# Kernel optimization log

Measured on AMD Instinct MI355X. Metric: run time of the kernel, lower is better.

Reference implementation:

```python
import jax, jax.numpy as jnp
import numpy as np

NEG_SLOPE = 0.2  # PyG GATConv default negative_slope
EPS = 1e-16


def gat_conv(x, src, dst, num_nodes, W, att_src, att_dst, bias, concat):
    """PyG-style GATConv (eval mode, no dropout). att_*: [H, C]."""
    H, C = att_src.shape
    h = (x @ W).reshape(num_nodes, H, C)                      # [N,H,C]
    a_s = jnp.einsum('nhc,hc->nh', h, att_src)                # [N,H]
    a_d = jnp.einsum('nhc,hc->nh', h, att_dst)                # [N,H]
    e = jax.nn.leaky_relu(a_s[src] + a_d[dst], NEG_SLOPE)     # [E,H]
    # segment softmax over edges grouped by destination node
    m = jax.lax.stop_gradient(jax.ops.segment_max(e, dst, num_segments=num_nodes))
    ex = jnp.exp(e - m[dst])
    denom = jax.ops.segment_sum(ex, dst, num_segments=num_nodes)
    alpha = ex / (denom[dst] + EPS)                           # [E,H]
    msg = h[src] * alpha[:, :, None]                          # [E,H,C]
    out = jax.ops.segment_sum(msg, dst, num_segments=num_nodes)  # [N,H,C]
    out = out.reshape(num_nodes, H * C) if concat else out.mean(axis=1)
    return out + bias


def setup_inputs() -> dict:
    key = jax.random.key(0)
    ks = jax.random.split(key, 12)
    N, E = 65536, 1310720
    IN, HID, OUT, HEADS = 768, 128, 2, 8
    C1 = HID // HEADS  # 16
    s = 0.05
    return {
        'x': jax.random.normal(ks[0], (N, IN), jnp.float32),
        'edge_index': jax.random.randint(ks[1], (2, E), 0, N, jnp.int64),
        'W1': jax.random.normal(ks[2], (IN, HEADS * C1), jnp.float32) * s,
        'att_src1': jax.random.normal(ks[3], (HEADS, C1), jnp.float32) * s,
        'att_dst1': jax.random.normal(ks[4], (HEADS, C1), jnp.float32) * s,
        'b1': jnp.zeros((HID,), jnp.float32),
        'Wp': jax.random.normal(ks[5], (IN, HID), jnp.float32) * s,
        'bp': jnp.zeros((HID,), jnp.float32),
        'W2': jax.random.normal(ks[6], (HID, OUT), jnp.float32) * s,
        'att_src2': jax.random.normal(ks[7], (1, OUT), jnp.float32) * s,
        'att_dst2': jax.random.normal(ks[8], (1, OUT), jnp.float32) * s,
        'b2': jnp.zeros((OUT,), jnp.float32),
    }


def reference(x, edge_index, W1, att_src1, att_dst1, b1, Wp, bp, W2, att_src2, att_dst2, b2):
    N = x.shape[0]
    loops = jnp.arange(N, dtype=edge_index.dtype)  # add_self_loops=True
    src = jnp.concatenate([edge_index[0], loops])
    dst = jnp.concatenate([edge_index[1], loops])
    # eval mode: dropout is identity
    h1 = gat_conv(x, src, dst, N, W1, att_src1, att_dst1, b1, concat=True)
    h = jax.nn.elu(h1 + x @ Wp + bp)  # residual projection + ELU
    return gat_conv(h, src, dst, N, W2, att_src2, att_dst2, b2, concat=False)
```

## Files before the change

### kernel.cpp

```cpp
#include <hip/hip_runtime.h>
#include <hip/hip_bf16.h>
#include <math.h>

#define NEG_SLOPE 0.2f

typedef __attribute__((ext_vector_type(8))) short short8;
typedef __attribute__((ext_vector_type(4))) float float4v;

__device__ __forceinline__ unsigned f2bf(float f) {
  unsigned u = __builtin_bit_cast(unsigned, f);
  return (u + 0x7fffu + ((u >> 16) & 1u)) >> 16;
}
__device__ __forceinline__ float bflo(unsigned u) {
  return __builtin_bit_cast(float, u << 16);
}
__device__ __forceinline__ float bfhi(unsigned u) {
  return __builtin_bit_cast(float, u & 0xffff0000u);
}
__device__ __forceinline__ unsigned cvtpk(float lo, float hi) {
  unsigned r;
  asm("v_cvt_pk_bf16_f32 %0, %1, %2" : "=v"(r) : "v"(lo), "v"(hi));
  return r;
}
__device__ __forceinline__ void gl2lds16(const void* g, void* l) {
  __builtin_amdgcn_global_load_lds(
      (const __attribute__((address_space(1))) unsigned*)g,
      (__attribute__((address_space(3))) unsigned*)l, 16, 0, 0);
}

__global__ __launch_bounds__(256) void convert_w(const float* __restrict__ W1,
                                                 const float* __restrict__ Wp,
                                                 short* __restrict__ Wt) {
  int k = blockIdx.x;
  int c = threadIdx.x;
  float v = (c < 128) ? W1[k * 128 + c] : Wp[k * 128 + (c - 128)];
  Wt[(size_t)c * 768 + k] = (short)f2bf(v);
}

__global__ __launch_bounds__(256, 4) void gemm_mfma(
    const float* __restrict__ x, const short* __restrict__ Wt,
    float* __restrict__ proj, unsigned* __restrict__ h1bf) {
  __shared__ short As[2][2048];
  __shared__ short Bs[2][8192];
  const int tid = threadIdx.x;
  const int w = tid >> 6, l = tid & 63;
  const int l15 = l & 15, l4 = l >> 4;
  const int row0 = blockIdx.x * 64;

  const float* xsrc = x + (size_t)(row0 + (tid >> 2)) * 768 + (tid & 3) * 8;
  const int awoff = (tid >> 2) * 64 + (((tid & 3) ^ ((tid >> 3) & 3)) << 4);
  const int aoff = l15 * 64 + ((l4 ^ ((l15 >> 1) & 3)) << 4);

  const char* bg[4];
#pragma unroll
  for (int i = 0; i < 4; i++) {
    int c = w * 64 + i * 16 + (l >> 2);
    int q = (l & 3) ^ ((l >> 3) & 3);
    bg[i] = (const char*)Wt + (size_t)c * 1536 + q * 16;
  }
  const int pc = l4 ^ ((l15 >> 1) & 3);

  float4v acc[4][4] = {};

  auto loadA = [&](int t, float4& r0, float4& r1) {
    const float* p = xsrc + t * 32;
    r0 = *(const float4*)p;
    r1 = *(const float4*)(p + 4);
  };
  auto writeA = [&](short* asb, const float4& r0, const float4& r1) {
    uint4 pk;
    pk.x = cvtpk(r0.x, r0.y);
    pk.y = cvtpk(r0.z, r0.w);
    pk.z = cvtpk(r1.x, r1.y);
    pk.w = cvtpk(r1.z, r1.w);
    *(uint4*)((char*)asb + awoff) = pk;
  };
  auto stageB = [&](short* bsb, int t) {
    gl2lds16(bg[0] + t * 64, (char*)bsb + w * 4096 + 0 * 1024);
    gl2lds16(bg[1] + t * 64, (char*)bsb + w * 4096 + 1 * 1024);
    gl2lds16(bg[2] + t * 64, (char*)bsb + w * 4096 + 2 * 1024);
    gl2lds16(bg[3] + t * 64, (char*)bsb + w * 4096 + 3 * 1024);
  };
  auto compute = [&](const short* asb, const short* bsb) {
    short8 afr[4];
#pragma unroll
    for (int rt = 0; rt < 4; rt++)
      afr[rt] = *(const short8*)((const char*)asb + rt * 1024 + aoff);
#pragma unroll
    for (int ct = 0; ct < 4; ct++) {
      short8 bfr =
          *(const short8*)((const char*)bsb + (w * 64 + ct * 16 + l15) * 64 + pc * 16);
#pragma unroll
      for (int rt = 0; rt < 4; rt++)
        acc[rt][ct] =
            __builtin_amdgcn_mfma_f32_16x16x32_bf16(afr[rt], bfr, acc[rt][ct], 0, 0, 0);
    }
  };

  float4 r0, r1;
  loadA(0, r0, r1);
  stageB(Bs[0], 0);
  writeA(As[0], r0, r1);
  __syncthreads();
  for (int t = 0; t < 24; t += 2) {
    loadA(t + 1, r0, r1);
    stageB(Bs[1], t + 1);
    compute(As[0], Bs[0]);
    writeA(As[1], r0, r1);
    __syncthreads();
    if (t + 2 < 24) {
      loadA(t + 2, r0, r1);
      stageB(Bs[0], t + 2);
    }
    compute(As[1], Bs[1]);
    if (t + 2 < 24) writeA(As[0], r0, r1);
    __syncthreads();
  }

  const int colbase = w * 64;
  if (w < 2) {
#pragma unroll
    for (int ct = 0; ct < 4; ct++) {
      const int c = colbase + ct * 16 + l15;
#pragma unroll
      for (int rt = 0; rt < 4; rt++) {
#pragma unroll
        for (int r = 0; r < 4; r++) {
          const int R = row0 + rt * 16 + l4 * 4 + r;
          unsigned u = f2bf(acc[rt][ct][r]);
          unsigned up = __shfl_xor(u, 1);
          if ((l15 & 1) == 0) h1bf[(size_t)R * 64 + (c >> 1)] = u | (up << 16);
        }
      }
    }
  } else {
#pragma unroll
    for (int ct = 0; ct < 4; ct++) {
      const int c = colbase - 128 + ct * 16 + l15;
#pragma unroll
      for (int rt = 0; rt < 4; rt++) {
#pragma unroll
        for (int r = 0; r < 4; r++) {
          const int R = row0 + rt * 16 + l4 * 4 + r;
          proj[(size_t)R * 128 + c] = acc[rt][ct][r];
        }
      }
    }
  }
}

__global__ __launch_bounds__(256) void attn1b(const uint4* __restrict__ h1bf4,
                                              const float* __restrict__ att_src1,
                                              const float* __restrict__ att_dst1,
                                              float* __restrict__ a_s1,
                                              float* __restrict__ a_d1) {
  const int t = blockIdx.x * 256 + threadIdx.x;
  const int n = t >> 3, h = t & 7;
  uint4 q0 = h1bf4[(size_t)n * 16 + h * 2];
  uint4 q1 = h1bf4[(size_t)n * 16 + h * 2 + 1];
  float v[16];
  v[0] = bflo(q0.x); v[1] = bfhi(q0.x); v[2] = bflo(q0.y); v[3] = bfhi(q0.y);
  v[4] = bflo(q0.z); v[5] = bfhi(q0.z); v[6] = bflo(q0.w); v[7] = bfhi(q0.w);
  v[8] = bflo(q1.x); v[9] = bfhi(q1.x); v[10] = bflo(q1.y); v[11] = bfhi(q1.y);
  v[12] = bflo(q1.z); v[13] = bfhi(q1.z); v[14] = bflo(q1.w); v[15] = bfhi(q1.w);
  float as = 0.f, ad = 0.f;
#pragma unroll
  for (int i = 0; i < 16; i++) {
    as += v[i] * att_src1[h * 16 + i];
    ad += v[i] * att_dst1[h * 16 + i];
  }
  a_s1[t] = as;
  a_d1[t] = ad;
}

__global__ void init_counts(int* counts, int N) {
  int i = blockIdx.x * blockDim.x + threadIdx.x;
  if (i < N) counts[i] = 1;
}

__global__ void hist_kernel(const int* __restrict__ dst, int* counts,
                            int* __restrict__ rank, int E) {
  int i = blockIdx.x * blockDim.x + threadIdx.x;
  int base = i * 4;
  if (base + 3 < E) {
    int4 d = *(const int4*)&dst[base];
    int4 r;
    r.x = atomicAdd(&counts[d.x], 1);
    r.y = atomicAdd(&counts[d.y], 1);
    r.z = atomicAdd(&counts[d.z], 1);
    r.w = atomicAdd(&counts[d.w], 1);
    *(int4*)&rank[base] = r;
  } else {
    for (int j = base; j < E; j++) rank[j] = atomicAdd(&counts[dst[j]], 1);
  }
}

__global__ __launch_bounds__(256) void scan_a(const int* __restrict__ counts,
                                              int* offsets, int* bsum) {
  __shared__ int s[256];
  int t = threadIdx.x, idx = blockIdx.x * 256 + t;
  int v = counts[idx];
  s[t] = v;
  __syncthreads();
  for (int d = 1; d < 256; d <<= 1) {
    int x = (t >= d) ? s[t - d] : 0;
    __syncthreads();
    s[t] += x;
    __syncthreads();
  }
  offsets[idx] = s[t] - v;
  if (t == 255) bsum[blockIdx.x] = s[t];
}

__global__ __launch_bounds__(256) void scan_b(int* bsum) {
  __shared__ int s[256];
  int t = threadIdx.x;
  int v = bsum[t];
  s[t] = v;
  __syncthreads();
  for (int d = 1; d < 256; d <<= 1) {
    int x = (t >= d) ? s[t - d] : 0;
    __syncthreads();
    s[t] += x;
    __syncthreads();
  }
  bsum[t] = s[t] - v;
}

__global__ __launch_bounds__(256) void scan_c(int* offsets, const int* bsum,
                                              int* sortedsrc, int N, int Etot) {
  int t = threadIdx.x, idx = blockIdx.x * 256 + t;
  int off = offsets[idx] + bsum[blockIdx.x];
  offsets[idx] = off;
  sortedsrc[off] = idx;
  if (idx == 0) offsets[N] = Etot;
}

__global__ void scatter_edges(const int* __restrict__ src,
                              const int* __restrict__ dst,
                              const int* __restrict__ rank,
                              const int* __restrict__ offsets,
                              int* __restrict__ sortedsrc, int E) {
  int i = blockIdx.x * blockDim.x + threadIdx.x;
  int base = i * 4;
  if (base + 3 < E) {
    int4 s = *(const int4*)&src[base];
    int4 d = *(const int4*)&dst[base];
    int4 r = *(const int4*)&rank[base];
    sortedsrc[offsets[d.x] + r.x] = s.x;
    sortedsrc[offsets[d.y] + r.y] = s.y;
    sortedsrc[offsets[d.z] + r.z] = s.z;
    sortedsrc[offsets[d.w] + r.w] = s.w;
  } else {
    for (int j = base; j < E; j++)
      sortedsrc[offsets[dst[j]] + rank[j]] = src[j];
  }
}

__global__ __launch_bounds__(256) void agg1_fused(
    const uint4* __restrict__ h1bf4, const float* __restrict__ proj,
    const float* __restrict__ a_s1, const float* __restrict__ a_d1,
    const int* __restrict__ offsets, const int* __restrict__ sortedsrc,
    const float* __restrict__ b1, const float* __restrict__ bp,
    const float* __restrict__ W2, const float* __restrict__ att_s2,
    const float* __restrict__ att_d2, float* __restrict__ h2,
    float* __restrict__ as2, float* __restrict__ ad2) {
  const int t = threadIdx.x;
  const int n = blockIdx.x * 16 + (t >> 4);
  const int k = t & 15;
  const int hd = k >> 1;
  const float ad = a_d1[n * 8 + hd];
  const int begin = offsets[n], end = offsets[n + 1];
  float acc[8] = {};
  float aw = 0.f;
  int j = begin;
  for (; j + 4 <= end; j += 4) {
    int s0 = sortedsrc[j], s1 = sortedsrc[j + 1];
    int s2 = sortedsrc[j + 2], s3 = sortedsrc[j + 3];
    float e0 = a_s1[s0 * 8 + hd], e1 = a_s1[s1 * 8 + hd];
    float e2 = a_s1[s2 * 8 + hd], e3 = a_s1[s3 * 8 + hd];
    uint4 q0 = h1bf4[(size_t)s0 * 16 + k];
    uint4 q1 = h1bf4[(size_t)s1 * 16 + k];
    uint4 q2 = h1bf4[(size_t)s2 * 16 + k];
    uint4 q3 = h1bf4[(size_t)s3 * 16 + k];
    e0 += ad; e1 += ad; e2 += ad; e3 += ad;
    float w0 = __expf(e0 > 0.f ? e0 : NEG_SLOPE * e0);
    float w1 = __expf(e1 > 0.f ? e1 : NEG_SLOPE * e1);
    float w2 = __expf(e2 > 0.f ? e2 : NEG_SLOPE * e2);
    float w3 = __expf(e3 > 0.f ? e3 : NEG_SLOPE * e3);
    acc[0] += w0 * bflo(q0.x) + w1 * bflo(q1.x) + w2 * bflo(q2.x) + w3 * bflo(q3.x);
    acc[1] += w0 * bfhi(q0.x) + w1 * bfhi(q1.x) + w2 * bfhi(q2.x) + w3 * bfhi(q3.x);
    acc[2] += w0 * bflo(q0.y) + w1 * bflo(q1.y) + w2 * bflo(q2.y) + w3 * bflo(q3.y);
    acc[3] += w0 * bfhi(q0.y) + w1 * bfhi(q1.y) + w2 * bfhi(q2.y) + w3 * bfhi(q3.y);
    acc[4] += w0 * bflo(q0.z) + w1 * bflo(q1.z) + w2 * bflo(q2.z) + w3 * bflo(q3.z);
    acc[5] += w0 * bfhi(q0.z) + w1 * bfhi(q1.z) + w2 * bfhi(q2.z) + w3 * bfhi(q3.z);
    acc[6] += w0 * bflo(q0.w) + w1 * bflo(q1.w) + w2 * bflo(q2.w) + w3 * bflo(q3.w);
    acc[7] += w0 * bfhi(q0.w) + w1 * bfhi(q1.w) + w2 * bfhi(q2.w) + w3 * bfhi(q3.w);
    aw += (w0 + w1) + (w2 + w3);
  }
  for (; j < end; j++) {
    int s0 = sortedsrc[j];
    float e0 = a_s1[s0 * 8 + hd] + ad;
    uint4 q0 = h1bf4[(size_t)s0 * 16 + k];
    float w0 = __expf(e0 > 0.f ? e0 : NEG_SLOPE * e0);
    acc[0] += w0 * bflo(q0.x);
    acc[1] += w0 * bfhi(q0.x);
    acc[2] += w0 * bflo(q0.y);
    acc[3] += w0 * bfhi(q0.y);
    acc[4] += w0 * bflo(q0.z);
    acc[5] += w0 * bfhi(q0.z);
    acc[6] += w0 * bflo(q0.w);
    acc[7] += w0 * bfhi(q0.w);
    aw += w0;
  }
  const float inv = 1.f / (aw + 1e-16f);
  const float4 pj0 = *(const float4*)&proj[(size_t)n * 128 + k * 8];
  const float4 pj1 = *(const float4*)&proj[(size_t)n * 128 + k * 8 + 4];
  const float4 b1a = *(const float4*)&b1[k * 8];
  const float4 b1b = *(const float4*)&b1[k * 8 + 4];
  const float4 bpa = *(const float4*)&bp[k * 8];
  const float4 bpb = *(const float4*)&bp[k * 8 + 4];
  float v[8];
  v[0] = acc[0] * inv + pj0.x + b1a.x + bpa.x;
  v[1] = acc[1] * inv + pj0.y + b1a.y + bpa.y;
  v[2] = acc[2] * inv + pj0.z + b1a.z + bpa.z;
  v[3] = acc[3] * inv + pj0.w + b1a.w + bpa.w;
  v[4] = acc[4] * inv + pj1.x + b1b.x + bpb.x;
  v[5] = acc[5] * inv + pj1.y + b1b.y + bpb.y;
  v[6] = acc[6] * inv + pj1.z + b1b.z + bpb.z;
  v[7] = acc[7] * inv + pj1.w + b1b.w + bpb.w;
  float p0 = 0.f, p1 = 0.f;
#pragma unroll
  for (int i = 0; i < 8; i++) {
    float vi = v[i] > 0.f ? v[i] : (__expf(v[i]) - 1.f);
    float2 w2 = *(const float2*)&W2[(k * 8 + i) * 2];
    p0 += vi * w2.x;
    p1 += vi * w2.y;
  }
#pragma unroll
  for (int off = 8; off; off >>= 1) {
    p0 += __shfl_xor(p0, off);
    p1 += __shfl_xor(p1, off);
  }
  if (k == 0) {
    h2[2 * n] = p0;
    h2[2 * n + 1] = p1;
    as2[n] = p0 * att_s2[0] + p1 * att_s2[1];
    ad2[n] = p0 * att_d2[0] + p1 * att_d2[1];
  }
}

__global__ __launch_bounds__(256) void agg2(
    const float* __restrict__ h2, const float* __restrict__ as2,
    const float* __restrict__ ad2, const int* __restrict__ offsets,
    const int* __restrict__ sortedsrc, const float* __restrict__ b2,
    float* __restrict__ out, int N) {
  const int node = blockIdx.x * 16 + (threadIdx.x >> 4);
  const int lane = threadIdx.x & 15;
  const int begin = offsets[node], end = offsets[node + 1];
  const float ad = ad2[node];
  float acc0 = 0.f, acc1 = 0.f, aw = 0.f;
  for (int j = begin + lane; j < end; j += 16) {
    int s = sortedsrc[j];
    float e = as2[s] + ad;
    float w = __expf(e > 0.f ? e : NEG_SLOPE * e);
    float2 hh = *(const float2*)&h2[2 * s];
    acc0 += w * hh.x;
    acc1 += w * hh.y;
    aw += w;
  }
#pragma unroll
  for (int off = 8; off; off >>= 1) {
    acc0 += __shfl_xor(acc0, off);
    acc1 += __shfl_xor(acc1, off);
    aw += __shfl_xor(aw, off);
  }
  if (lane == 0) {
    float inv = 1.f / (aw + 1e-16f);
    out[2 * node] = acc0 * inv + b2[0];
    out[2 * node + 1] = acc1 * inv + b2[1];
  }
}

extern "C" void kernel_launch(void* const* d_in, const int* in_sizes, int n_in,
                              void* d_out, int out_size, void* d_ws,
                              size_t ws_size, hipStream_t stream) {
  const float* x = (const float*)d_in[0];
  const int* edge_index = (const int*)d_in[1];
  const float* W1 = (const float*)d_in[2];
  const float* att_src1 = (const float*)d_in[3];
  const float* att_dst1 = (const float*)d_in[4];
  const float* b1 = (const float*)d_in[5];
  const float* Wp = (const float*)d_in[6];
  const float* bp = (const float*)d_in[7];
  const float* W2 = (const float*)d_in[8];
  const float* att_src2 = (const float*)d_in[9];
  const float* att_dst2 = (const float*)d_in[10];
  const float* b2 = (const float*)d_in[11];
  float* out = (float*)d_out;

  const int N = in_sizes[0] / 768;
  const int E = in_sizes[1] / 2;
  const int Etot = E + N;
  const int* src = edge_index;
  const int* dst = edge_index + E;

  char* ws = (char*)d_ws;
  size_t off = 0;
  auto alloc = [&](size_t bytes) {
    size_t cur = off;
    off += (bytes + 255) & ~(size_t)255;
    return (void*)(ws + cur);
  };
  float* proj = (float*)alloc((size_t)N * 128 * 4);
  unsigned* h1bf = (unsigned*)alloc((size_t)N * 64 * 4);
  float* a_s1 = (float*)alloc((size_t)N * 8 * 4);
  float* a_d1 = (float*)alloc((size_t)N * 8 * 4);
  float* h2 = (float*)alloc((size_t)N * 2 * 4);
  float* as2 = (float*)alloc((size_t)N * 4);
  float* ad2 = (float*)alloc((size_t)N * 4);
  int* counts = (int*)alloc((size_t)N * 4);
  int* offsets = (int*)alloc(((size_t)N + 1) * 4);
  int* rank = (int*)alloc((size_t)E * 4);
  int* bsum = (int*)alloc(256 * 4);
  int* sortedsrc = (int*)alloc((size_t)Etot * 4);
  short* Wt = (short*)alloc((size_t)256 * 768 * 2);

  convert_w<<<768, 256, 0, stream>>>(W1, Wp, Wt);
  gemm_mfma<<<N / 64, 256, 0, stream>>>(x, Wt, proj, h1bf);
  attn1b<<<N * 8 / 256, 256, 0, stream>>>((const uint4*)h1bf, att_src1,
                                          att_dst1, a_s1, a_d1);
  init_counts<<<(N + 255) / 256, 256, 0, stream>>>(counts, N);
  hist_kernel<<<(E / 4 + 255) / 256, 256, 0, stream>>>(dst, counts, rank, E);
  scan_a<<<N / 256, 256, 0, stream>>>(counts, offsets, bsum);
  scan_b<<<1, 256, 0, stream>>>(bsum);
  scan_c<<<N / 256, 256, 0, stream>>>(offsets, bsum, sortedsrc, N, Etot);
  scatter_edges<<<(E / 4 + 255) / 256, 256, 0, stream>>>(src, dst, rank,
                                                         offsets, sortedsrc, E);
  agg1_fused<<<N / 16, 256, 0, stream>>>((const uint4*)h1bf, proj, a_s1, a_d1,
                                         offsets, sortedsrc, b1, bp, W2,
                                         att_src2, att_dst2, h2, as2, ad2);
  agg2<<<N / 16, 256, 0, stream>>>(h2, as2, ad2, offsets, sortedsrc, b2, out,
                                   N);
}
```

Measured before the change: 500.9 us.

## Double GEMM row tile to 128 with 8 waves; pack layer-2 node data into float4

The GEMM block now covers 128 rows with 512 threads arranged as 2x4 waves, so each B tile staged into LDS is shared by twice as many rows. This halves the per-wave B staging and raises LDS use per block. Separately, the layer-2 per-node values (h2 pair, a_s, a_d) are packed into one float4 record. Each gathered edge in agg2 then needs a single 16-byte load instead of separate scattered loads.

```diff
diff --git a/kernel.cpp b/kernel.cpp
--- a/kernel.cpp
+++ b/kernel.cpp
@@ -37,24 +37,25 @@
   Wt[(size_t)c * 768 + k] = (short)f2bf(v);
 }
 
-__global__ __launch_bounds__(256, 4) void gemm_mfma(
+__global__ __launch_bounds__(512, 4) void gemm_mfma(
     const float* __restrict__ x, const short* __restrict__ Wt,
     float* __restrict__ proj, unsigned* __restrict__ h1bf) {
-  __shared__ short As[2][2048];
+  __shared__ short As[2][4096];
   __shared__ short Bs[2][8192];
   const int tid = threadIdx.x;
   const int w = tid >> 6, l = tid & 63;
+  const int wr = w >> 2, wc = w & 3;
   const int l15 = l & 15, l4 = l >> 4;
-  const int row0 = blockIdx.x * 64;
+  const int row0 = blockIdx.x * 128;
 
   const float* xsrc = x + (size_t)(row0 + (tid >> 2)) * 768 + (tid & 3) * 8;
   const int awoff = (tid >> 2) * 64 + (((tid & 3) ^ ((tid >> 3) & 3)) << 4);
-  const int aoff = l15 * 64 + ((l4 ^ ((l15 >> 1) & 3)) << 4);
-
-  const char* bg[4];
-#pragma unroll
-  for (int i = 0; i < 4; i++) {
-    int c = w * 64 + i * 16 + (l >> 2);
+  const int aoff = (wr * 64 + l15) * 64 + ((l4 ^ ((l15 >> 1) & 3)) << 4);
+
+  const char* bg[2];
+#pragma unroll
+  for (int i = 0; i < 2; i++) {
+    int c = w * 32 + i * 16 + (l >> 2);
     int q = (l & 3) ^ ((l >> 3) & 3);
     bg[i] = (const char*)Wt + (size_t)c * 1536 + q * 16;
   }
@@ -76,10 +77,8 @@
     *(uint4*)((char*)asb + awoff) = pk;
   };
   auto stageB = [&](short* bsb, int t) {
-    gl2lds16(bg[0] + t * 64, (char*)bsb + w * 4096 + 0 * 1024);
-    gl2lds16(bg[1] + t * 64, (char*)bsb + w * 4096 + 1 * 1024);
-    gl2lds16(bg[2] + t * 64, (char*)bsb + w * 4096 + 2 * 1024);
-    gl2lds16(bg[3] + t * 64, (char*)bsb + w * 4096 + 3 * 1024);
+    gl2lds16(bg[0] + t * 64, (char*)bsb + w * 2048 + 0 * 1024);
+    gl2lds16(bg[1] + t * 64, (char*)bsb + w * 2048 + 1 * 1024);
   };
   auto compute = [&](const short* asb, const short* bsb) {
     short8 afr[4];
@@ -89,7 +88,7 @@
 #pragma unroll
     for (int ct = 0; ct < 4; ct++) {
       short8 bfr =
-          *(const short8*)((const char*)bsb + (w * 64 + ct * 16 + l15) * 64 + pc * 16);
+          *(const short8*)((const char*)bsb + (wc * 64 + ct * 16 + l15) * 64 + pc * 16);
 #pragma unroll
       for (int rt = 0; rt < 4; rt++)
         acc[rt][ct] =
@@ -117,16 +116,15 @@
     __syncthreads();
   }
 
-  const int colbase = w * 64;
-  if (w < 2) {
+  if (wc < 2) {
 #pragma unroll
     for (int ct = 0; ct < 4; ct++) {
-      const int c = colbase + ct * 16 + l15;
+      const int c = wc * 64 + ct * 16 + l15;
 #pragma unroll
       for (int rt = 0; rt < 4; rt++) {
 #pragma unroll
         for (int r = 0; r < 4; r++) {
-          const int R = row0 + rt * 16 + l4 * 4 + r;
+          const int R = row0 + wr * 64 + rt * 16 + l4 * 4 + r;
           unsigned u = f2bf(acc[rt][ct][r]);
           unsigned up = __shfl_xor(u, 1);
           if ((l15 & 1) == 0) h1bf[(size_t)R * 64 + (c >> 1)] = u | (up << 16);
@@ -136,12 +134,12 @@
   } else {
 #pragma unroll
     for (int ct = 0; ct < 4; ct++) {
-      const int c = colbase - 128 + ct * 16 + l15;
+      const int c = (wc - 2) * 64 + ct * 16 + l15;
 #pragma unroll
       for (int rt = 0; rt < 4; rt++) {
 #pragma unroll
         for (int r = 0; r < 4; r++) {
-          const int R = row0 + rt * 16 + l4 * 4 + r;
+          const int R = row0 + wr * 64 + rt * 16 + l4 * 4 + r;
           proj[(size_t)R * 128 + c] = acc[rt][ct][r];
         }
       }
@@ -263,8 +261,7 @@
     const int* __restrict__ offsets, const int* __restrict__ sortedsrc,
     const float* __restrict__ b1, const float* __restrict__ bp,
     const float* __restrict__ W2, const float* __restrict__ att_s2,
-    const float* __restrict__ att_d2, float* __restrict__ h2,
-    float* __restrict__ as2, float* __restrict__ ad2) {
+    const float* __restrict__ att_d2, float4* __restrict__ rec) {
   const int t = threadIdx.x;
   const int n = blockIdx.x * 16 + (t >> 4);
   const int k = t & 15;
@@ -343,30 +340,28 @@
     p1 += __shfl_xor(p1, off);
   }
   if (k == 0) {
-    h2[2 * n] = p0;
-    h2[2 * n + 1] = p1;
-    as2[n] = p0 * att_s2[0] + p1 * att_s2[1];
-    ad2[n] = p0 * att_d2[0] + p1 * att_d2[1];
+    float as = p0 * att_s2[0] + p1 * att_s2[1];
+    float adv = p0 * att_d2[0] + p1 * att_d2[1];
+    rec[n] = make_float4(p0, p1, as, adv);
   }
 }
 
 __global__ __launch_bounds__(256) void agg2(
-    const float* __restrict__ h2, const float* __restrict__ as2,
-    const float* __restrict__ ad2, const int* __restrict__ offsets,
+    const float4* __restrict__ rec, const int* __restrict__ offsets,
     const int* __restrict__ sortedsrc, const float* __restrict__ b2,
     float* __restrict__ out, int N) {
   const int node = blockIdx.x * 16 + (threadIdx.x >> 4);
   const int lane = threadIdx.x & 15;
   const int begin = offsets[node], end = offsets[node + 1];
-  const float ad = ad2[node];
+  const float ad = rec[node].w;
   float acc0 = 0.f, acc1 = 0.f, aw = 0.f;
   for (int j = begin + lane; j < end; j += 16) {
     int s = sortedsrc[j];
-    float e = as2[s] + ad;
+    float4 rs = rec[s];
+    float e = rs.z + ad;
     float w = __expf(e > 0.f ? e : NEG_SLOPE * e);
-    float2 hh = *(const float2*)&h2[2 * s];
-    acc0 += w * hh.x;
-    acc1 += w * hh.y;
+    acc0 += w * rs.x;
+    acc1 += w * rs.y;
     aw += w;
   }
 #pragma unroll
@@ -416,9 +411,7 @@
   unsigned* h1bf = (unsigned*)alloc((size_t)N * 64 * 4);
   float* a_s1 = (float*)alloc((size_t)N * 8 * 4);
   float* a_d1 = (float*)alloc((size_t)N * 8 * 4);
-  float* h2 = (float*)alloc((size_t)N * 2 * 4);
-  float* as2 = (float*)alloc((size_t)N * 4);
-  float* ad2 = (float*)alloc((size_t)N * 4);
+  float4* rec = (float4*)alloc((size_t)N * 16);
   int* counts = (int*)alloc((size_t)N * 4);
   int* offsets = (int*)alloc(((size_t)N + 1) * 4);
   int* rank = (int*)alloc((size_t)E * 4);
@@ -427,7 +420,7 @@
   short* Wt = (short*)alloc((size_t)256 * 768 * 2);
 
   convert_w<<<768, 256, 0, stream>>>(W1, Wp, Wt);
-  gemm_mfma<<<N / 64, 256, 0, stream>>>(x, Wt, proj, h1bf);
+  gemm_mfma<<<N / 128, 512, 0, stream>>>(x, Wt, proj, h1bf);
   attn1b<<<N * 8 / 256, 256, 0, stream>>>((const uint4*)h1bf, att_src1,
                                           att_dst1, a_s1, a_d1);
   init_counts<<<(N + 255) / 256, 256, 0, stream>>>(counts, N);
@@ -439,7 +432,6 @@
                                                          offsets, sortedsrc, E);
   agg1_fused<<<N / 16, 256, 0, stream>>>((const uint4*)h1bf, proj, a_s1, a_d1,
                                          offsets, sortedsrc, b1, bp, W2,
-                                         att_src2, att_dst2, h2, as2, ad2);
-  agg2<<<N / 16, 256, 0, stream>>>(h2, as2, ad2, offsets, sortedsrc, b2, out,
-                                   N);
-}
+                                         att_src2, att_dst2, rec);
+  agg2<<<N / 16, 256, 0, stream>>>(rec, offsets, sortedsrc, b2, out, N);
+}
```

Result: no change. 493.4 us (-1.5%).
